# Kernel tuning notes

Hardware: AMD Instinct MI355X
Metric: run time of the kernel (lower is better)

Reference implementation:

```python
import jax, jax.numpy as jnp
import numpy as np

T, D, H = 2048, 1024, 16
HS = D // H  # head_size = 64
DFF = 4 * D
LN_EPS = 1e-6


def layernorm(x, scale, bias, eps=LN_EPS):
    mu = jnp.mean(x, axis=-1, keepdims=True)
    var = jnp.mean(jnp.square(x - mu), axis=-1, keepdims=True)
    return (x - mu) * jax.lax.rsqrt(var + eps) * scale + bias


def setup_inputs() -> dict:
    key = jax.random.key(0)
    ks = jax.random.split(key, 12)
    s_in = 1.0 / np.sqrt(D)
    s_ff = 1.0 / np.sqrt(DFF)
    return {
        "x": jax.random.normal(ks[0], (T, D), jnp.float32),
        "Wq": jax.random.normal(ks[1], (H, D, HS), jnp.float32) * s_in,
        "Wk": jax.random.normal(ks[2], (H, D, HS), jnp.float32) * s_in,
        "Wv": jax.random.normal(ks[3], (H, D, HS), jnp.float32) * s_in,
        "Wo": jax.random.normal(ks[4], (D, D), jnp.float32) * s_in,
        "bo": jnp.zeros((D,), jnp.float32),
        "W1": jax.random.normal(ks[5], (D, DFF), jnp.float32) * s_in,
        "b1": jnp.zeros((DFF,), jnp.float32),
        "W2": jax.random.normal(ks[6], (DFF, D), jnp.float32) * s_ff,
        "b2": jnp.zeros((D,), jnp.float32),
        "ln1_scale": jnp.ones((D,), jnp.float32),
        "ln1_bias": jnp.zeros((D,), jnp.float32),
        "ln2_scale": jnp.ones((D,), jnp.float32),
        "ln2_bias": jnp.zeros((D,), jnp.float32),
        "training": 0,
    }


def reference(x, Wq, Wk, Wv, Wo, bo, W1, b1, W2, b2,
              ln1_scale, ln1_bias, ln2_scale, ln2_bias, training):
    # --- pre-LN causal multi-head self-attention ---
    h = layernorm(x, ln1_scale, ln1_bias)
    q = jnp.einsum("td,hdk->htk", h, Wq)  # [H,T,HS]
    k = jnp.einsum("td,hdk->htk", h, Wk)
    v = jnp.einsum("td,hdk->htk", h, Wv)
    scores = jnp.einsum("htk,hsk->hts", q, k) / jnp.sqrt(jnp.float32(HS))
    causal = jnp.tril(jnp.ones((T, T), jnp.float32))
    scores = jnp.where(causal == 0, -jnp.inf, scores)
    wei = jax.nn.softmax(scores, axis=-1)
    av = jnp.einsum("hts,hsk->htk", wei, v)          # [H,T,HS]
    av = av.transpose(1, 0, 2).reshape(T, H * HS)    # concat over heads
    x = x + av @ Wo + bo                              # dropout deterministic -> identity
    # --- pre-LN feed-forward ---
    h2 = layernorm(x, ln2_scale, ln2_bias)
    ff = jax.nn.relu(h2 @ W1 + b1) @ W2 + b2
    x = x + ff
    return x
```

## Files before the change

kernel.cpp:

```cpp
#include <hip/hip_runtime.h>
#include <cstdint>


typedef __bf16 bf16;
typedef __bf16 bf16x4 __attribute__((ext_vector_type(4)));
typedef __bf16 bf16x8 __attribute__((ext_vector_type(8)));
typedef float floatx4 __attribute__((ext_vector_type(4)));

__device__ __forceinline__ void ld_g2l(const bf16* g, bf16* l) {
    __builtin_amdgcn_global_load_lds(
        (const __attribute__((address_space(1))) void*)g,
        (__attribute__((address_space(3))) void*)l, 16, 0, 0);
}

__device__ __forceinline__ void ln_row_body(
    const float* __restrict__ x, const float* __restrict__ sc,
    const float* __restrict__ bi, bf16* __restrict__ out,
    int row, int tid, float* wred)
{
    const float4 v = ((const float4*)(x + (size_t)row * 1024))[tid];
    float s1 = v.x + v.y + v.z + v.w;
    float s2 = v.x * v.x + v.y * v.y + v.z * v.z + v.w * v.w;
#pragma unroll
    for (int mm = 1; mm < 64; mm <<= 1) {
        s1 += __shfl_xor(s1, mm);
        s2 += __shfl_xor(s2, mm);
    }
    const int wave = tid >> 6, lane = tid & 63;
    if (lane == 0) { wred[wave] = s1; wred[4 + wave] = s2; }
    __syncthreads();
    s1 = wred[0] + wred[1] + wred[2] + wred[3];
    s2 = wred[4] + wred[5] + wred[6] + wred[7];
    const float mu = s1 * (1.f / 1024.f);
    const float var = fmaxf(s2 * (1.f / 1024.f) - mu * mu, 0.f);
    const float rr = rsqrtf(var + 1e-6f);
    const float4 scv = ((const float4*)sc)[tid];
    const float4 biv = ((const float4*)bi)[tid];
    bf16x4 ov;
    ov[0] = (bf16)((v.x - mu) * rr * scv.x + biv.x);
    ov[1] = (bf16)((v.y - mu) * rr * scv.y + biv.y);
    ov[2] = (bf16)((v.z - mu) * rr * scv.z + biv.z);
    ov[3] = (bf16)((v.w - mu) * rr * scv.w + biv.w);
    *(bf16x4*)(out + (size_t)row * 1024 + tid * 4) = ov;
}

__global__ __launch_bounds__(256) void prep_kernel(
    const float* __restrict__ Wq, const float* __restrict__ Wk,
    const float* __restrict__ Wv, bf16* __restrict__ Wqkvt,
    const float* __restrict__ Wo, bf16* __restrict__ Wot,
    const float* __restrict__ W1, bf16* __restrict__ W1t,
    const float* __restrict__ W2, bf16* __restrict__ W2t,
    const float* __restrict__ x, const float* __restrict__ ln1s,
    const float* __restrict__ ln1b, bf16* __restrict__ hbuf)
{
    __shared__ float tile[64][65];
    __shared__ float wred[8];
    const int b = blockIdx.x;
    const int tid = threadIdx.x;

    if (b >= 3072) {
        ln_row_body(x, ln1s, ln1b, hbuf, b - 3072, tid, wred);
        return;
    }

    const int tx = tid & 63, ty = tid >> 6;
    const float* src; bf16* dst; int R, C, c0, r0;
    if (b < 768) {
        const int sec = b >> 4, ti = b & 15;
        const int m = sec >> 4, h = sec & 15;
        src = (m == 0 ? Wq : (m == 1 ? Wk : Wv)) + h * 65536;
        dst = Wqkvt + m * 1048576 + h * 65536;
        R = 1024; C = 64; c0 = 0; r0 = ti * 64;
    } else if (b < 1024) {
        const int i = b - 768;
        src = Wo; dst = Wot; R = 1024; C = 1024;
        c0 = (i & 15) * 64; r0 = (i >> 4) * 64;
    } else if (b < 2048) {
        const int i = b - 1024;
        src = W1; dst = W1t; R = 1024; C = 4096;
        c0 = (i & 63) * 64; r0 = (i >> 6) * 64;
    } else {
        const int i = b - 2048;
        src = W2; dst = W2t; R = 4096; C = 1024;
        c0 = (i & 15) * 64; r0 = (i >> 4) * 64;
    }
#pragma unroll
    for (int i = ty; i < 64; i += 4)
        tile[i][tx] = src[(size_t)(r0 + i) * C + c0 + tx];
    __syncthreads();
#pragma unroll
    for (int i = ty; i < 64; i += 4)
        dst[(size_t)(c0 + i) * R + r0 + tx] = (bf16)tile[tx][i];
}

__global__ __launch_bounds__(256) void ln_kernel(
    const float* __restrict__ x, const float* __restrict__ sc,
    const float* __restrict__ bi, bf16* __restrict__ out)
{
    __shared__ float wred[8];
    ln_row_body(x, sc, bi, out, blockIdx.x, threadIdx.x, wred);
}

__global__ __launch_bounds__(256) void transpose_head_kernel(
    const bf16* __restrict__ qkv, bf16* __restrict__ dst, int colOff)
{
    __shared__ bf16 tile[32][33];
    const int tx = threadIdx.x, ty = threadIdx.y;
    const int h = blockIdx.z;
    const int j0 = blockIdx.x * 32, s0 = blockIdx.y * 32;
#pragma unroll
    for (int i = ty; i < 32; i += 8)
        tile[i][tx] = qkv[(size_t)(s0 + i) * 3072 + colOff + h * 64 + j0 + tx];
    __syncthreads();
#pragma unroll
    for (int i = ty; i < 32; i += 8)
        dst[(size_t)h * 64 * 2048 + (size_t)(j0 + i) * 2048 + s0 + tx] = tile[tx][i];
}

__global__ __launch_bounds__(256) void reduce4_kernel(
    const float* __restrict__ p, const float* __restrict__ bias,
    const float* __restrict__ res, float* __restrict__ out)
{
    const int idx = blockIdx.x * 256 + threadIdx.x;
    const int c4 = idx & 255;
    const float4 a0 = ((const float4*)p)[idx];
    const float4 a1 = ((const float4*)(p + 2097152))[idx];
    const float4 a2 = ((const float4*)(p + 4194304))[idx];
    const float4 a3 = ((const float4*)(p + 6291456))[idx];
    const float4 bi = ((const float4*)bias)[c4];
    const float4 r = ((const float4*)res)[idx];
    float4 o;
    o.x = (a0.x + a1.x) + (a2.x + a3.x) + bi.x + r.x;
    o.y = (a0.y + a1.y) + (a2.y + a3.y) + bi.y + r.y;
    o.z = (a0.z + a1.z) + (a2.z + a3.z) + bi.z + r.z;
    o.w = (a0.w + a1.w) + (a2.w + a3.w) + bi.w + r.w;
    ((float4*)out)[idx] = o;
}

template <int MODE, int NG, int MG, int SPLITK>
__global__ __launch_bounds__(256) void gemm128_kernel(
    const bf16* __restrict__ A, const bf16* __restrict__ Bt,
    int N, int K,
    float* __restrict__ outF, bf16* __restrict__ outB,
    const float* __restrict__ bias)
{
    __shared__ __align__(16) bf16 Alds[2][128][64];
    __shared__ __align__(16) bf16 Blds[2][128][64];
    const int tid  = threadIdx.x;
    const int lane = tid & 63;
    const int w    = tid >> 6;
    const int r15  = lane & 15;
    const int quad = lane >> 4;

    const int id    = blockIdx.x + gridDim.x * (blockIdx.y + gridDim.y * blockIdx.z);
    const int xcd   = id & 7;
    const int seq   = id >> 3;
    const int nPerX = gridDim.x / NG;
    const int mPerX = gridDim.y / MG;
    const int nm    = nPerX * mPerX;
    const int z     = seq / nm;
    const int loc   = seq - z * nm;
    const int bn    = ((xcd % NG) * nPerX + (loc % nPerX)) * 128;
    const int bm    = ((xcd / NG) * mPerX + (loc / nPerX)) * 128;

    const int wm = (w >> 1) * 64;
    const int wn = (w & 1) * 64;

    floatx4 acc[4][4];
#pragma unroll
    for (int i = 0; i < 4; ++i)
#pragma unroll
        for (int j = 0; j < 4; ++j) acc[i][j] = (floatx4)(0.f);

    const int KS    = K / SPLITK;
    const int kBase = (SPLITK > 1) ? z * KS : 0;
    const int nIter = KS / 64;

    const int lrow = lane >> 3;
    const int gch  = (lane & 7) ^ lrow;
    const bf16* aptr = A + (size_t)(bm + w * 16 + lrow) * K + kBase + gch * 8;
    const bf16* bptr = Bt + (size_t)(bn + w * 16 + lrow) * K + kBase + gch * 8;

#pragma unroll
    for (int rr = 0; rr < 2; ++rr)
#pragma unroll
        for (int t = 0; t < 2; ++t) {
            ld_g2l(aptr + (size_t)(rr * 64 + t * 8) * K, &Alds[0][rr * 64 + w * 16 + t * 8][0]);
            ld_g2l(bptr + (size_t)(rr * 64 + t * 8) * K, &Blds[0][rr * 64 + w * 16 + t * 8][0]);
        }

    for (int it = 0; it < nIter; ++it) {
        const int buf = it & 1;
        __syncthreads();
        if (it + 1 < nIter) {
            const int k2 = (it + 1) * 64;
#pragma unroll
            for (int rr = 0; rr < 2; ++rr)
#pragma unroll
                for (int t = 0; t < 2; ++t) {
                    ld_g2l(aptr + (size_t)(rr * 64 + t * 8) * K + k2,
                           &Alds[buf ^ 1][rr * 64 + w * 16 + t * 8][0]);
                    ld_g2l(bptr + (size_t)(rr * 64 + t * 8) * K + k2,
                           &Blds[buf ^ 1][rr * 64 + w * 16 + t * 8][0]);
                }
        }
#pragma unroll
        for (int kk = 0; kk < 2; ++kk) {
            const int pc = ((kk * 4 + quad) ^ (r15 & 7)) * 8;
            bf16x8 af[4], bfr[4];
#pragma unroll
            for (int i = 0; i < 4; ++i)
                af[i] = *(const bf16x8*)(&Alds[buf][wm + i * 16 + r15][pc]);
#pragma unroll
            for (int j = 0; j < 4; ++j)
                bfr[j] = *(const bf16x8*)(&Blds[buf][wn + j * 16 + r15][pc]);
#pragma unroll
            for (int i = 0; i < 4; ++i)
#pragma unroll
                for (int j = 0; j < 4; ++j)
                    acc[i][j] = __builtin_amdgcn_mfma_f32_16x16x32_bf16(
                        af[i], bfr[j], acc[i][j], 0, 0, 0);
        }
    }

    const int row0 = bm + wm + quad * 4;
    const int col0 = bn + wn + r15;
    float* po = (MODE == 3) ? outF + (size_t)z * 2048 * 1024 : outF;
#pragma unroll
    for (int i = 0; i < 4; ++i) {
#pragma unroll
        for (int reg = 0; reg < 4; ++reg) {
            const int row = row0 + i * 16 + reg;
#pragma unroll
            for (int j = 0; j < 4; ++j) {
                const int col = col0 + j * 16;
                float v = acc[i][j][reg];
                if (MODE == 0) {
                    outB[(size_t)row * N + col] = (bf16)v;
                } else if (MODE == 2) {
                    v += bias[col];
                    outB[(size_t)row * N + col] = (bf16)fmaxf(v, 0.f);
                } else {
                    po[(size_t)row * N + col] = v;
                }
            }
        }
    }
}

template <int NG, int MG>
__global__ __launch_bounds__(256) void gemm64_kernel(
    const bf16* __restrict__ A, const bf16* __restrict__ Bt,
    int N, int K,
    float* __restrict__ outF, const float* __restrict__ bias,
    const float* __restrict__ res)
{
    __shared__ __align__(16) bf16 Alds[2][64][64];
    __shared__ __align__(16) bf16 Blds[2][64][64];
    const int tid  = threadIdx.x;
    const int lane = tid & 63;
    const int w    = tid >> 6;
    const int r15  = lane & 15;
    const int quad = lane >> 4;

    const int id    = blockIdx.x + gridDim.x * blockIdx.y;
    const int xcd   = id & 7;
    const int seq   = id >> 3;
    const int nPerX = gridDim.x / NG;
    const int mPerX = gridDim.y / MG;
    const int loc   = seq % (nPerX * mPerX);
    const int bn    = ((xcd % NG) * nPerX + (loc % nPerX)) * 64;
    const int bm    = ((xcd / NG) * mPerX + (loc / nPerX)) * 64;

    const int wm = (w >> 1) * 32;
    const int wn = (w & 1) * 32;

    floatx4 acc[2][2];
#pragma unroll
    for (int i = 0; i < 2; ++i)
#pragma unroll
        for (int j = 0; j < 2; ++j) acc[i][j] = (floatx4)(0.f);

    const int nIter = K / 64;
    const int lrow = lane >> 3;
    const int gch  = (lane & 7) ^ lrow;
    const bf16* aptr = A + (size_t)(bm + w * 16 + lrow) * K + gch * 8;
    const bf16* bptr = Bt + (size_t)(bn + w * 16 + lrow) * K + gch * 8;

#pragma unroll
    for (int t = 0; t < 2; ++t) {
        ld_g2l(aptr + (size_t)t * 8 * K, &Alds[0][w * 16 + t * 8][0]);
        ld_g2l(bptr + (size_t)t * 8 * K, &Blds[0][w * 16 + t * 8][0]);
    }

    for (int it = 0; it < nIter; ++it) {
        const int buf = it & 1;
        __syncthreads();
        if (it + 1 < nIter) {
            const int k2 = (it + 1) * 64;
#pragma unroll
            for (int t = 0; t < 2; ++t) {
                ld_g2l(aptr + (size_t)t * 8 * K + k2, &Alds[buf ^ 1][w * 16 + t * 8][0]);
                ld_g2l(bptr + (size_t)t * 8 * K + k2, &Blds[buf ^ 1][w * 16 + t * 8][0]);
            }
        }
#pragma unroll
        for (int kk = 0; kk < 2; ++kk) {
            const int pc = ((kk * 4 + quad) ^ (r15 & 7)) * 8;
            bf16x8 af[2], bfr[2];
#pragma unroll
            for (int i = 0; i < 2; ++i)
                af[i] = *(const bf16x8*)(&Alds[buf][wm + i * 16 + r15][pc]);
#pragma unroll
            for (int j = 0; j < 2; ++j)
                bfr[j] = *(const bf16x8*)(&Blds[buf][wn + j * 16 + r15][pc]);
#pragma unroll
            for (int i = 0; i < 2; ++i)
#pragma unroll
                for (int j = 0; j < 2; ++j)
                    acc[i][j] = __builtin_amdgcn_mfma_f32_16x16x32_bf16(
                        af[i], bfr[j], acc[i][j], 0, 0, 0);
        }
    }

    const int row0 = bm + wm + quad * 4;
    const int col0 = bn + wn + r15;
#pragma unroll
    for (int i = 0; i < 2; ++i)
#pragma unroll
        for (int reg = 0; reg < 4; ++reg) {
            const int row = row0 + i * 16 + reg;
#pragma unroll
            for (int j = 0; j < 2; ++j) {
                const int col = col0 + j * 16;
                outF[(size_t)row * N + col] =
                    acc[i][j][reg] + bias[col] + res[(size_t)row * N + col];
            }
        }
}

__global__ __launch_bounds__(256) void attn_kernel(
    const bf16* __restrict__ qkv, const bf16* __restrict__ vt,
    bf16* __restrict__ out)
{
    __shared__ __align__(16) bf16 Qs[64][64];
    __shared__ __align__(16) bf16 Ks[2][64][64];
    __shared__ __align__(16) bf16 Vs[2][64][64];
    __shared__ __align__(16) bf16 Ps[4][16][72];

    const int tid  = threadIdx.x;
    const int w    = tid >> 6;
    const int lane = tid & 63;
    const int r15  = lane & 15;
    const int quad = lane >> 4;
    const int rl   = lane >> 3;
    const int gsw  = (lane & 7) ^ (rl & 7);

    const int idp = blockIdx.x + 16 * blockIdx.y;
    const int seq = idp >> 3;
    const int h   = (idp & 7) * 2 + (seq & 1);
    const int qp  = seq >> 1;
    const int qt  = blockIdx.z ? 31 - qp : qp;
    const int qrow0 = qt * 64;

    const bf16* qsec = qkv + h * 64;
    const bf16* ksec = qkv + 1024 + h * 64;
    const bf16* vth  = vt + (size_t)h * 64 * 2048;

#pragma unroll
    for (int t = 0; t < 2; ++t) {
        const int r = t * 32 + w * 8 + rl;
        ld_g2l(qsec + (size_t)(qrow0 + r) * 3072 + gsw * 8, &Qs[t * 32 + w * 8][0]);
        ld_g2l(ksec + (size_t)r * 3072 + gsw * 8, &Ks[0][t * 32 + w * 8][0]);
        ld_g2l(vth + (size_t)r * 2048 + gsw * 8, &Vs[0][t * 32 + w * 8][0]);
    }
    __syncthreads();

    bf16x8 qf[2];
#pragma unroll
    for (int c = 0; c < 2; ++c) {
        const int p = ((c * 4 + quad) ^ (r15 & 7)) * 8;
        qf[c] = *(const bf16x8*)&Qs[w * 16 + r15][p];
    }

    float lacc[4] = {0.f, 0.f, 0.f, 0.f};
    floatx4 O[4];
#pragma unroll
    for (int j = 0; j < 4; ++j) O[j] = (floatx4)(0.f);

#pragma unroll 1
    for (int sb = 0; sb <= qt; ++sb) {
        const int buf = sb & 1;
        if (sb < qt) {
            const int s1 = (sb + 1) * 64;
#pragma unroll
            for (int t = 0; t < 2; ++t) {
                const int r = t * 32 + w * 8 + rl;
                ld_g2l(ksec + (size_t)(s1 + r) * 3072 + gsw * 8, &Ks[buf ^ 1][t * 32 + w * 8][0]);
                ld_g2l(vth + (size_t)r * 2048 + s1 + gsw * 8, &Vs[buf ^ 1][t * 32 + w * 8][0]);
            }
        }

        floatx4 S[4];
#pragma unroll
        for (int j = 0; j < 4; ++j) S[j] = (floatx4)(0.f);
#pragma unroll
        for (int c = 0; c < 2; ++c) {
#pragma unroll
            for (int j = 0; j < 4; ++j) {
                const int p = ((c * 4 + quad) ^ (r15 & 7)) * 8;
                const bf16x8 b = *(const bf16x8*)&Ks[buf][j * 16 + r15][p];
                S[j] = __builtin_amdgcn_mfma_f32_16x16x32_bf16(qf[c], b, S[j], 0, 0, 0);
            }
        }
        const bool diag = (sb == qt);
        const int rowl = w * 16 + quad * 4;
#pragma unroll
        for (int j = 0; j < 4; ++j) {
            const int col = j * 16 + r15;
#pragma unroll
            for (int r = 0; r < 4; ++r) {
                float p = exp2f(fmaf(S[j][r], 0.18033688f, -28.853901f));
                if (diag && col > rowl + r) p = 0.f;
                S[j][r] = p;
                lacc[r] += p;
            }
        }
#pragma unroll
        for (int r = 0; r < 4; ++r)
#pragma unroll
            for (int j = 0; j < 4; ++j)
                Ps[w][quad * 4 + r][j * 16 + r15] = (bf16)S[j][r];
#pragma unroll
        for (int c = 0; c < 2; ++c) {
            const bf16x8 a = *(const bf16x8*)&Ps[w][r15][c * 32 + quad * 8];
#pragma unroll
            for (int j = 0; j < 4; ++j) {
                const int p = ((c * 4 + quad) ^ (r15 & 7)) * 8;
                const bf16x8 b = *(const bf16x8*)&Vs[buf][j * 16 + r15][p];
                O[j] = __builtin_amdgcn_mfma_f32_16x16x32_bf16(a, b, O[j], 0, 0, 0);
            }
        }
        __syncthreads();
    }
#pragma unroll
    for (int r = 0; r < 4; ++r) {
#pragma unroll
        for (int d = 1; d < 16; d <<= 1) lacc[r] += __shfl_xor(lacc[r], d);
    }
#pragma unroll
    for (int r = 0; r < 4; ++r) {
        const float inv = 1.0f / lacc[r];
        const int row = qrow0 + w * 16 + quad * 4 + r;
#pragma unroll
        for (int j = 0; j < 4; ++j)
            out[(size_t)row * 1024 + h * 64 + j * 16 + r15] = (bf16)(O[j][r] * inv);
    }
}

extern "C" void kernel_launch(void* const* d_in, const int* in_sizes, int n_in,
                              void* d_out, int out_size, void* d_ws, size_t ws_size,
                              hipStream_t stream)
{
    const float* x    = (const float*)d_in[0];
    const float* Wq   = (const float*)d_in[1];
    const float* Wk   = (const float*)d_in[2];
    const float* Wv   = (const float*)d_in[3];
    const float* Wo   = (const float*)d_in[4];
    const float* bo   = (const float*)d_in[5];
    const float* W1   = (const float*)d_in[6];
    const float* b1   = (const float*)d_in[7];
    const float* W2   = (const float*)d_in[8];
    const float* b2   = (const float*)d_in[9];
    const float* ln1s = (const float*)d_in[10];
    const float* ln1b = (const float*)d_in[11];
    const float* ln2s = (const float*)d_in[12];
    const float* ln2b = (const float*)d_in[13];

    char* ws = (char*)d_ws;
    bf16*  Wqkvt = (bf16*)(ws + 0);
    bf16*  Wot   = (bf16*)(ws + 6291456);
    bf16*  W1t   = (bf16*)(ws + 8388608);
    bf16*  W2t   = (bf16*)(ws + 16777216);
    bf16*  hbuf  = (bf16*)(ws + 25165824);
    bf16*  QKV   = (bf16*)(ws + 29360128);
    bf16*  Vt    = (bf16*)(ws + 41943040);
    bf16*  Obuf  = (bf16*)(ws + 46137344);
    float* x1    = (float*)(ws + 50331648);
    bf16*  h2    = (bf16*)(ws + 58720256);
    bf16*  ff1   = (bf16*)(ws + 62914560);
    float* psum  = (float*)(ws + 79691776);

    const dim3 tb(32, 8);

    prep_kernel<<<5120, 256, 0, stream>>>(Wq, Wk, Wv, Wqkvt, Wo, Wot,
                                          W1, W1t, W2, W2t,
                                          x, ln1s, ln1b, hbuf);
    gemm128_kernel<0,4,2,1><<<dim3(24, 16), 256, 0, stream>>>(hbuf, Wqkvt, 3072, 1024, nullptr, QKV, nullptr);
    transpose_head_kernel<<<dim3(2, 64, 16), tb, 0, stream>>>(QKV, Vt, 2048);
    attn_kernel<<<dim3(16, 16, 2), 256, 0, stream>>>(QKV, Vt, Obuf);
    gemm64_kernel<4,2><<<dim3(16, 32), 256, 0, stream>>>(Obuf, Wot, 1024, 1024, x1, bo, x);
    ln_kernel<<<2048, 256, 0, stream>>>(x1, ln2s, ln2b, h2);
    gemm128_kernel<2,4,2,1><<<dim3(32, 16), 256, 0, stream>>>(h2, W1t, 4096, 1024, nullptr, ff1, b1);
    gemm128_kernel<3,2,4,4><<<dim3(8, 16, 4), 256, 0, stream>>>(ff1, W2t, 1024, 4096, psum, nullptr, nullptr);
    reduce4_kernel<<<2048, 256, 0, stream>>>(psum, b2, x1, (float*)d_out);
}
```

Baseline: 250.9 us.

## Split attention key range into two halves with separate combine kernel

Each causal query tile's key blocks are split across two workgroups, doubling the grid to raise parallelism. Each half writes unnormalized bf16 partial outputs and row sums, and a new combine kernel adds them and normalizes. MFMA sections are also wrapped with raised wave priority. This costs an extra launch, extra global traffic, and bf16 rounding of partial sums.

```diff
diff --git a/kernel.cpp b/kernel.cpp
--- a/kernel.cpp
+++ b/kernel.cpp
@@ -341,7 +341,7 @@
 
 __global__ __launch_bounds__(256) void attn_kernel(
     const bf16* __restrict__ qkv, const bf16* __restrict__ vt,
-    bf16* __restrict__ out)
+    bf16* __restrict__ Opart, float* __restrict__ Lpart)
 {
     __shared__ __align__(16) bf16 Qs[64][64];
     __shared__ __align__(16) bf16 Ks[2][64][64];
@@ -356,23 +356,40 @@
     const int rl   = lane >> 3;
     const int gsw  = (lane & 7) ^ (rl & 7);
 
-    const int idp = blockIdx.x + 16 * blockIdx.y;
-    const int seq = idp >> 3;
-    const int h   = (idp & 7) * 2 + (seq & 1);
-    const int qp  = seq >> 1;
-    const int qt  = blockIdx.z ? 31 - qp : qp;
+    const int b    = blockIdx.x;
+    const int idp  = b & 255;
+    const int seq  = idp >> 3;
+    const int h    = (idp & 7) * 2 + (seq & 1);
+    const int qp   = seq >> 1;
+    const int qt   = ((b >> 8) & 1) ? 31 - qp : qp;
+    const int half = b >> 9;
     const int qrow0 = qt * 64;
+
+    const int n0    = (qt + 2) >> 1;
+    const int sbBeg = half ? n0 : 0;
+    const int sbEnd = half ? qt + 1 : n0;
+
+    const int tile = half * 512 + h * 32 + qt;
+    const size_t obase = (size_t)tile * 4096;
+
+    if (sbBeg >= sbEnd) {
+        const int4 z = {0, 0, 0, 0};
+        ((int4*)(Opart + obase))[tid] = z;
+        if (tid < 64) Lpart[tile * 64 + tid] = 0.f;
+        return;
+    }
 
     const bf16* qsec = qkv + h * 64;
     const bf16* ksec = qkv + 1024 + h * 64;
     const bf16* vth  = vt + (size_t)h * 64 * 2048;
+    const int s0 = sbBeg * 64;
 
 #pragma unroll
     for (int t = 0; t < 2; ++t) {
         const int r = t * 32 + w * 8 + rl;
         ld_g2l(qsec + (size_t)(qrow0 + r) * 3072 + gsw * 8, &Qs[t * 32 + w * 8][0]);
-        ld_g2l(ksec + (size_t)r * 3072 + gsw * 8, &Ks[0][t * 32 + w * 8][0]);
-        ld_g2l(vth + (size_t)r * 2048 + gsw * 8, &Vs[0][t * 32 + w * 8][0]);
+        ld_g2l(ksec + (size_t)(s0 + r) * 3072 + gsw * 8, &Ks[0][t * 32 + w * 8][0]);
+        ld_g2l(vth + (size_t)r * 2048 + s0 + gsw * 8, &Vs[0][t * 32 + w * 8][0]);
     }
     __syncthreads();
 
@@ -388,10 +405,11 @@
 #pragma unroll
     for (int j = 0; j < 4; ++j) O[j] = (floatx4)(0.f);
 
+    int ns = 0;
 #pragma unroll 1
-    for (int sb = 0; sb <= qt; ++sb) {
-        const int buf = sb & 1;
-        if (sb < qt) {
+    for (int sb = sbBeg; sb < sbEnd; ++sb, ++ns) {
+        const int buf = ns & 1;
+        if (sb + 1 < sbEnd) {
             const int s1 = (sb + 1) * 64;
 #pragma unroll
             for (int t = 0; t < 2; ++t) {
@@ -404,15 +422,17 @@
         floatx4 S[4];
 #pragma unroll
         for (int j = 0; j < 4; ++j) S[j] = (floatx4)(0.f);
+        __builtin_amdgcn_s_setprio(1);
 #pragma unroll
         for (int c = 0; c < 2; ++c) {
 #pragma unroll
             for (int j = 0; j < 4; ++j) {
                 const int p = ((c * 4 + quad) ^ (r15 & 7)) * 8;
-                const bf16x8 b = *(const bf16x8*)&Ks[buf][j * 16 + r15][p];
-                S[j] = __builtin_amdgcn_mfma_f32_16x16x32_bf16(qf[c], b, S[j], 0, 0, 0);
-            }
-        }
+                const bf16x8 kb = *(const bf16x8*)&Ks[buf][j * 16 + r15][p];
+                S[j] = __builtin_amdgcn_mfma_f32_16x16x32_bf16(qf[c], kb, S[j], 0, 0, 0);
+            }
+        }
+        __builtin_amdgcn_s_setprio(0);
         const bool diag = (sb == qt);
         const int rowl = w * 16 + quad * 4;
 #pragma unroll
@@ -431,16 +451,18 @@
 #pragma unroll
             for (int j = 0; j < 4; ++j)
                 Ps[w][quad * 4 + r][j * 16 + r15] = (bf16)S[j][r];
+        __builtin_amdgcn_s_setprio(1);
 #pragma unroll
         for (int c = 0; c < 2; ++c) {
             const bf16x8 a = *(const bf16x8*)&Ps[w][r15][c * 32 + quad * 8];
 #pragma unroll
             for (int j = 0; j < 4; ++j) {
                 const int p = ((c * 4 + quad) ^ (r15 & 7)) * 8;
-                const bf16x8 b = *(const bf16x8*)&Vs[buf][j * 16 + r15][p];
-                O[j] = __builtin_amdgcn_mfma_f32_16x16x32_bf16(a, b, O[j], 0, 0, 0);
-            }
-        }
+                const bf16x8 vb = *(const bf16x8*)&Vs[buf][j * 16 + r15][p];
+                O[j] = __builtin_amdgcn_mfma_f32_16x16x32_bf16(a, vb, O[j], 0, 0, 0);
+            }
+        }
+        __builtin_amdgcn_s_setprio(0);
         __syncthreads();
     }
 #pragma unroll
@@ -450,12 +472,43 @@
     }
 #pragma unroll
     for (int r = 0; r < 4; ++r) {
-        const float inv = 1.0f / lacc[r];
-        const int row = qrow0 + w * 16 + quad * 4 + r;
+        const int row = w * 16 + quad * 4 + r;
 #pragma unroll
         for (int j = 0; j < 4; ++j)
-            out[(size_t)row * 1024 + h * 64 + j * 16 + r15] = (bf16)(O[j][r] * inv);
-    }
+            Opart[obase + (size_t)row * 64 + j * 16 + r15] = (bf16)(O[j][r]);
+    }
+    if (r15 == 0) {
+#pragma unroll
+        for (int r = 0; r < 4; ++r)
+            Lpart[tile * 64 + w * 16 + quad * 4 + r] = lacc[r];
+    }
+}
+
+__global__ __launch_bounds__(256) void attn_combine_kernel(
+    const bf16* __restrict__ Op, const float* __restrict__ Lp,
+    bf16* __restrict__ out)
+{
+    const int b = blockIdx.x;
+    const int h = b >> 5, qt = b & 31;
+    const int tid = threadIdx.x;
+    const int r = tid >> 2, cg = tid & 3;
+    const size_t pa = (size_t)b * 4096 + r * 64 + cg * 16;
+    const bf16x8 a0 = *(const bf16x8*)(Op + pa);
+    const bf16x8 a1 = *(const bf16x8*)(Op + pa + 8);
+    const bf16x8 b0 = *(const bf16x8*)(Op + 2097152 + pa);
+    const bf16x8 b1 = *(const bf16x8*)(Op + 2097152 + pa + 8);
+    const float la = Lp[b * 64 + r];
+    const float lb = Lp[32768 + b * 64 + r];
+    const float inv = 1.f / (la + lb);
+    bf16x8 o0, o1;
+#pragma unroll
+    for (int i = 0; i < 8; ++i) {
+        o0[i] = (bf16)(((float)a0[i] + (float)b0[i]) * inv);
+        o1[i] = (bf16)(((float)a1[i] + (float)b1[i]) * inv);
+    }
+    bf16* dst = out + (size_t)(qt * 64 + r) * 1024 + h * 64 + cg * 16;
+    *(bf16x8*)dst = o0;
+    *(bf16x8*)(dst + 8) = o1;
 }
 
 extern "C" void kernel_launch(void* const* d_in, const int* in_sizes, int n_in,
@@ -490,6 +543,8 @@
     bf16*  h2    = (bf16*)(ws + 58720256);
     bf16*  ff1   = (bf16*)(ws + 62914560);
     float* psum  = (float*)(ws + 79691776);
+    bf16*  Opart = (bf16*)(ws + 79691776);
+    float* Lpart = (float*)(ws + 88080384);
 
     const dim3 tb(32, 8);
 
@@ -498,7 +553,8 @@
                                           x, ln1s, ln1b, hbuf);
     gemm128_kernel<0,4,2,1><<<dim3(24, 16), 256, 0, stream>>>(hbuf, Wqkvt, 3072, 1024, nullptr, QKV, nullptr);
     transpose_head_kernel<<<dim3(2, 64, 16), tb, 0, stream>>>(QKV, Vt, 2048);
-    attn_kernel<<<dim3(16, 16, 2), 256, 0, stream>>>(QKV, Vt, Obuf);
+    attn_kernel<<<1024, 256, 0, stream>>>(QKV, Vt, Opart, Lpart);
+    attn_combine_kernel<<<512, 256, 0, stream>>>(Opart, Lpart, Obuf);
     gemm64_kernel<4,2><<<dim3(16, 32), 256, 0, stream>>>(Obuf, Wot, 1024, 1024, x1, bo, x);
     ln_kernel<<<2048, 256, 0, stream>>>(x1, ln2s, ln2b, h2);
     gemm128_kernel<2,4,2,1><<<dim3(32, 16), 256, 0, stream>>>(h2, W1t, 4096, 1024, nullptr, ff1, b1);
```

New measurement: 251.9 us. Within noise of the previous version (+0.4%).
